# Kernel tuning notes

Hardware: AMD Instinct MI355X
Metric: run time of the kernel (lower is better)

The kernel has to match this reference:

```python
import jax, jax.numpy as jnp
import numpy as np

N_LAYERS, B, H, D = 24, 16, 32, 64
E = H * D            # 2048
TS_H = 32            # token_shift_hidden_dim
N_BRANCH = 5         # key, receptance, decay, value, bonus
GN_EPS = 1e-3        # keras GroupNormalization default epsilon


def setup_inputs() -> dict:
    key = jax.random.key(0)
    ks = jax.random.split(key, 20)
    s = 0.02
    return {
        "inputs": jax.random.normal(ks[0], (B, E), jnp.float32),
        "state": jax.random.normal(ks[1], (N_LAYERS, 1, B, E), jnp.float32),
        "state_matrix": jax.random.normal(ks[2], (N_LAYERS, B, H, D, D), jnp.float32),
        # stacked branch params, order: key, receptance, decay, value, bonus
        "mus": jax.random.normal(ks[3], (N_BRANCH, E), jnp.float32) * s,
        "lambdas": jax.random.normal(ks[4], (N_BRANCH, E), jnp.float32) * s,
        "Aw": jax.random.normal(ks[5], (N_BRANCH, E, TS_H), jnp.float32) * s,
        "Ab": jnp.zeros((N_BRANCH, TS_H), jnp.float32),
        "Bw": jax.random.normal(ks[6], (N_BRANCH, TS_H, E), jnp.float32) * s,
        "Bb": jnp.zeros((N_BRANCH, E), jnp.float32),
        "MW": jax.random.normal(ks[7], (N_BRANCH, H, D, D), jnp.float32) * s,
        "Mb": jnp.zeros((N_BRANCH, H, D), jnp.float32),
        "gate_mu": jax.random.normal(ks[8], (E,), jnp.float32) * s,
        "gate_W": jax.random.normal(ks[9], (E, E), jnp.float32) * s,
        "gate_b": jnp.zeros((E,), jnp.float32),
        "gn_gamma": jnp.ones((E,), jnp.float32),
        "gn_beta": jnp.zeros((E,), jnp.float32),
        "out_W": jax.random.normal(ks[10], (E, E), jnp.float32) * s,
        "out_b": jnp.zeros((E,), jnp.float32),
        "layer_id": 12,
    }


def reference(inputs, state, state_matrix, mus, lambdas, Aw, Ab, Bw, Bb, MW, Mb,
              gate_mu, gate_W, gate_b, gn_gamma, gn_beta, out_W, out_b, layer_id):
    x = inputs                       # [B, E]
    last_x = state[layer_id, 0]      # [B, E]
    diff = x - last_x

    # ddlerp token shift for all 5 branches at once:
    # lora(x + diff*mu) = lambda + tanh(. @ A) @ B ; out = x + lora * diff
    lora_in = x[None] + diff[None] * mus[:, None]                      # [5, B, E]
    hdn = jnp.tanh(jnp.einsum('sbe,seh->sbh', lora_in, Aw) + Ab[:, None])
    lora = jnp.einsum('sbh,she->sbe', hdn, Bw) + Bb[:, None] + lambdas[:, None]
    ts = (lora * diff[None] + x[None]).reshape(N_BRANCH, B, H, D)      # [5, B, H, D]

    # per-head dense for each branch
    proj = jnp.einsum('sbhd,shde->sbhe', ts, MW) + Mb[:, None]         # [5, B, H, D]
    k, r, w_raw, v, u = proj[0], proj[1], proj[2], proj[3], proj[4]

    g = (x * gate_mu + last_x * (1.0 - gate_mu)) @ gate_W + gate_b     # [B, E]

    kv = k[..., :, None] * v[..., None, :]                             # [B, H, D, D]
    w = jnp.exp(-jnp.exp(w_raw))[..., None]                            # [B, H, D, 1]
    S = state_matrix[layer_id]                                         # [B, H, D, D]
    wkv = kv * u[..., None] + S
    new_S = w * S + kv
    rwkv = jnp.einsum('bhij,bhj->bhi', wkv, r)                         # [B, H, D]

    # group norm: num_heads groups over channel axis
    mean = rwkv.mean(-1, keepdims=True)
    var = rwkv.var(-1, keepdims=True)
    normed = ((rwkv - mean) / jnp.sqrt(var + GN_EPS)).reshape(B, E)
    normed = normed * gn_gamma + gn_beta

    time_mixed = (normed * jax.nn.silu(g)) @ out_W + out_b             # [B, E]

    new_state = state.at[layer_id, 0].set(inputs)
    new_state_matrix = state_matrix.at[layer_id].set(new_S)
    return time_mixed, new_state, new_state_matrix
```

## Files before the change

### kernel.cpp

```cpp
#include <hip/hip_runtime.h>
#include <math.h>

#define NL 24
#define BB 16
#define HH 32
#define DD 64
#define EE 2048
#define TSH 32
#define NB 5
#define BE (BB*EE)
#define STATE_N (NL*BB*EE)
#define SM_N (NL*BB*HH*DD*DD)
#define GN_EPS 1e-3f

__global__ void k_prep(const float4* __restrict__ state4, const float4* __restrict__ inputs4,
                       float4* __restrict__ out4, const int* __restrict__ lid_p,
                       float* __restrict__ out_tm, float* __restrict__ g,
                       const float* __restrict__ out_b, const float* __restrict__ gate_b) {
    int blk = blockIdx.x, tid = threadIdx.x;
    if (blk < 768) {
        int i = blk * 256 + tid;
        int lid = *lid_p;
        int lo = lid * (BE / 4);
        float4 v = (i >= lo && i < lo + BE / 4) ? inputs4[i - lo] : state4[i];
        out4[i] = v;
    } else {
        int idx = (blk - 768) * 256 + tid;
        if (idx < BE) out_tm[idx] = out_b[idx & (EE - 1)];
        else g[idx - BE] = gate_b[(idx - BE) & (EE - 1)];
    }
}

__global__ void k_hdn(const float* __restrict__ inputs, const float* __restrict__ state,
                      const float* __restrict__ mus, const float* __restrict__ Aw,
                      const float* __restrict__ Ab, float* __restrict__ hdn,
                      const int* __restrict__ lid_p) {
    int s = blockIdx.x / BB, b = blockIdx.x % BB;
    int tid = threadIdx.x;
    int lid = *lid_p;
    __shared__ float li[EE];
    const float* x  = inputs + b * EE;
    const float* lx = state + lid * BE + b * EE;
    const float* mu = mus + s * EE;
    for (int e = tid; e < EE; e += 256) {
        float xv = x[e];
        li[e] = xv + (xv - lx[e]) * mu[e];
    }
    __syncthreads();
    int h = tid & 31, part = tid >> 5;
    const float* A = Aw + s * EE * TSH;
    float acc = 0.f;
    int e0 = part * 256;
    for (int e = e0; e < e0 + 256; ++e) acc += li[e] * A[e * TSH + h];
    __shared__ float red[32][9];
    red[h][part] = acc;
    __syncthreads();
    if (tid < 32) {
        float sum = Ab[s * TSH + tid];
        #pragma unroll
        for (int p = 0; p < 8; ++p) sum += red[tid][p];
        hdn[(s * BB + b) * TSH + tid] = tanhf(sum);
    }
}

__global__ void k_ts(const float* __restrict__ inputs, const float* __restrict__ state,
                     const float* __restrict__ lambdas, const float* __restrict__ Bw,
                     const float* __restrict__ Bb, const float* __restrict__ hdn,
                     const float* __restrict__ gate_mu, float* __restrict__ ts,
                     float* __restrict__ gx, const int* __restrict__ lid_p) {
    int idx = blockIdx.x * 256 + threadIdx.x;
    int s = idx / BE, r = idx % BE;
    int b = r / EE, e = r % EE;
    int lid = *lid_p;
    const float* hp = hdn + (s * BB + b) * TSH;
    const float* Bp = Bw + s * TSH * EE + e;
    float acc = Bb[s * EE + e] + lambdas[s * EE + e];
    #pragma unroll
    for (int h = 0; h < TSH; ++h) acc += hp[h] * Bp[h * EE];
    float xv = inputs[r];
    float lxv = state[lid * BE + r];
    ts[idx] = acc * (xv - lxv) + xv;
    if (s == 0) {
        float gm = gate_mu[e];
        gx[r] = xv * gm + lxv * (1.f - gm);
    }
}

__global__ void k_proj(const float* __restrict__ ts, const float* __restrict__ MW,
                       const float* __restrict__ Mb, float* __restrict__ proj) {
    int bi = blockIdx.x;
    int s = bi / (BB * 8);
    int r = bi % (BB * 8);
    int b = r / 8, hg = r % 8;
    int q = threadIdx.x >> 6, e = threadIdx.x & 63;
    int h = hg * 4 + q;
    __shared__ float tl[4][DD];
    tl[q][e] = ts[((s * BB + b) * HH + h) * DD + e];
    __syncthreads();
    const float* M = MW + (s * HH + h) * DD * DD;
    float acc = Mb[(s * HH + h) * DD + e];
    #pragma unroll 8
    for (int d = 0; d < DD; ++d) acc += tl[q][d] * M[d * DD + e];
    proj[((s * BB + b) * HH + h) * DD + e] = acc;
}

__global__ void k_mm(const float* __restrict__ Arows, const float* __restrict__ W,
                     float* out) {
    int et = blockIdx.x & 15, kc = blockIdx.x >> 4;
    int e = et * 128 + threadIdx.x;
    int k0 = kc * 64;
    float acc[BB];
    #pragma unroll
    for (int b = 0; b < BB; ++b) acc[b] = 0.f;
    #pragma unroll 4
    for (int kk = 0; kk < 64; ++kk) {
        float wv = W[(k0 + kk) * EE + e];
        #pragma unroll
        for (int b = 0; b < BB; ++b) acc[b] += Arows[b * EE + k0 + kk] * wv;
    }
    #pragma unroll
    for (int b = 0; b < BB; ++b) atomicAdd(&out[b * EE + e], acc[b]);
}

__global__ void k_sm_rwkv(const float4* __restrict__ sm4, float4* __restrict__ out4,
                          const float* __restrict__ proj, const float* __restrict__ g,
                          const float* __restrict__ gn_gamma, const float* __restrict__ gn_beta,
                          float* __restrict__ a_out, const int* __restrict__ lid_p) {
    int blk = blockIdx.x;
    int tid = threadIdx.x;
    int lid = *lid_p;
    int layer = blk / (BB * HH);
    int base4 = blk * (DD * DD / 4);
    if (layer != lid) {
        const float4* src = sm4 + base4;
        float4* dst = out4 + base4;
        #pragma unroll
        for (int p = 0; p < 4; ++p) dst[p * 256 + tid] = src[p * 256 + tid];
        return;
    }
    int r = blk % (BB * HH);
    int b = r / HH, h = r % HH;
    int j = tid & 63, q = tid >> 6;
    const float* P = proj + (b * HH + h) * DD + j;
    float kv   = P[0 * BE];
    float rv   = P[1 * BE];
    float wraw = P[2 * BE];
    float vv   = P[3 * BE];
    float uv   = P[4 * BE];
    float wv = expf(-expf(wraw));
    float vr = vv * rv;
    #pragma unroll
    for (int o = 32; o; o >>= 1) vr += __shfl_xor(vr, o);
    __shared__ float rw[DD];
    const float* S = (const float*)(sm4 + base4);
    float* NS = (float*)(out4 + base4);
    for (int ii = 0; ii < 16; ii += 4) {
        int i0 = q * 16 + ii;
        float sv[4], kk[4], ww[4], uu[4], pp[4];
        #pragma unroll
        for (int t = 0; t < 4; ++t) {
            sv[t] = S[(i0 + t) * DD + j];
            kk[t] = __shfl(kv, i0 + t);
            ww[t] = __shfl(wv, i0 + t);
            uu[t] = __shfl(uv, i0 + t);
        }
        #pragma unroll
        for (int t = 0; t < 4; ++t) {
            NS[(i0 + t) * DD + j] = ww[t] * sv[t] + kk[t] * vv;
            pp[t] = sv[t] * rv;
        }
        #pragma unroll
        for (int o = 32; o; o >>= 1) {
            #pragma unroll
            for (int t = 0; t < 4; ++t) pp[t] += __shfl_xor(pp[t], o);
        }
        if (j == 0) {
            #pragma unroll
            for (int t = 0; t < 4; ++t) rw[i0 + t] = kk[t] * uu[t] * vr + pp[t];
        }
    }
    __syncthreads();
    if (tid < DD) {
        float x = rw[tid];
        float m = x;
        #pragma unroll
        for (int o = 32; o; o >>= 1) m += __shfl_xor(m, o);
        m *= (1.f / 64.f);
        float d = x - m;
        float var = d * d;
        #pragma unroll
        for (int o = 32; o; o >>= 1) var += __shfl_xor(var, o);
        var *= (1.f / 64.f);
        float normed = d * rsqrtf(var + GN_EPS);
        int e = h * DD + tid;
        float ng = normed * gn_gamma[e] + gn_beta[e];
        float gval = g[b * EE + e];
        float silu = gval / (1.f + expf(-gval));
        a_out[b * EE + e] = ng * silu;
    }
}

extern "C" void kernel_launch(void* const* d_in, const int* in_sizes, int n_in,
                              void* d_out, int out_size, void* d_ws, size_t ws_size,
                              hipStream_t stream) {
    const float* inputs   = (const float*)d_in[0];
    const float* state    = (const float*)d_in[1];
    const float* sm       = (const float*)d_in[2];
    const float* mus      = (const float*)d_in[3];
    const float* lambdas  = (const float*)d_in[4];
    const float* Aw       = (const float*)d_in[5];
    const float* Ab       = (const float*)d_in[6];
    const float* Bw       = (const float*)d_in[7];
    const float* Bb       = (const float*)d_in[8];
    const float* MW       = (const float*)d_in[9];
    const float* Mb       = (const float*)d_in[10];
    const float* gate_mu  = (const float*)d_in[11];
    const float* gate_W   = (const float*)d_in[12];
    const float* gate_b   = (const float*)d_in[13];
    const float* gn_gamma = (const float*)d_in[14];
    const float* gn_beta  = (const float*)d_in[15];
    const float* out_W    = (const float*)d_in[16];
    const float* out_b    = (const float*)d_in[17];
    const int*   lid      = (const int*)d_in[18];

    float* out_tm    = (float*)d_out;
    float* out_state = out_tm + BE;
    float* out_sm    = out_state + STATE_N;

    float* ws   = (float*)d_ws;
    float* ts   = ws;
    float* proj = ts + NB * BE;
    float* hdn  = proj + NB * BE;
    float* gx   = hdn + NB * BB * TSH;
    float* g    = gx + BE;
    float* a    = g + BE;

    k_prep<<<1024, 256, 0, stream>>>((const float4*)state, (const float4*)inputs,
                                     (float4*)out_state, lid, out_tm, g, out_b, gate_b);
    k_hdn<<<NB * BB, 256, 0, stream>>>(inputs, state, mus, Aw, Ab, hdn, lid);
    k_ts<<<(NB * BE) / 256, 256, 0, stream>>>(inputs, state, lambdas, Bw, Bb, hdn,
                                              gate_mu, ts, gx, lid);
    k_proj<<<NB * BB * 8, 256, 0, stream>>>(ts, MW, Mb, proj);
    k_mm<<<512, 128, 0, stream>>>(gx, gate_W, g);
    k_sm_rwkv<<<NL * BB * HH, 256, 0, stream>>>(
        (const float4*)sm, (float4*)out_sm, proj, g, gn_gamma, gn_beta, a, lid);
    k_mm<<<512, 128, 0, stream>>>(a, out_W, out_tm);
}
```

Measured before the change: 442.4 us.

## Fuse seven launches into three and overlap state copy with matmuls

Merges the hdn, token-shift and per-head projection stages into a single per-(branch,batch) block inside the head kernel, keeping the intermediates in shared memory. The gate matmul now runs inside the same launch as the active-layer RWKV update. The bulk copy of the 23 untouched state-matrix layers moves into the tail launch beside the output matmul, and SiLU gating moves into that matmul's shared-memory staging of A. The matmuls also stage the activation rows in LDS. This removes launch gaps and lets the big memory copy overlap compute, but the fused head stage runs only 80 blocks doing serial work.

Measured after the change: 470.5 us. +6.3%, slower.

```diff
diff --git a/kernel.cpp b/kernel.cpp
--- a/kernel.cpp
+++ b/kernel.cpp
@@ -13,133 +13,136 @@
 #define SM_N (NL*BB*HH*DD*DD)
 #define GN_EPS 1e-3f
 
-__global__ void k_prep(const float4* __restrict__ state4, const float4* __restrict__ inputs4,
-                       float4* __restrict__ out4, const int* __restrict__ lid_p,
-                       float* __restrict__ out_tm, float* __restrict__ g,
-                       const float* __restrict__ out_b, const float* __restrict__ gate_b) {
+__global__ __launch_bounds__(256) void k_head(
+    const float4* __restrict__ state4, const float4* __restrict__ inputs4,
+    float4* __restrict__ out_state4,
+    float* __restrict__ out_tm, float* __restrict__ g,
+    const float* __restrict__ out_b, const float* __restrict__ gate_b,
+    const float* __restrict__ inputs, const float* __restrict__ state,
+    const float* __restrict__ mus, const float* __restrict__ Aw,
+    const float* __restrict__ Ab, const float* __restrict__ lambdas,
+    const float* __restrict__ Bw, const float* __restrict__ Bb,
+    const float* __restrict__ MW, const float* __restrict__ Mb,
+    const float* __restrict__ gate_mu, float* __restrict__ proj,
+    float* __restrict__ gx, const int* __restrict__ lid_p)
+{
     int blk = blockIdx.x, tid = threadIdx.x;
+    int lid = *lid_p;
     if (blk < 768) {
         int i = blk * 256 + tid;
-        int lid = *lid_p;
         int lo = lid * (BE / 4);
         float4 v = (i >= lo && i < lo + BE / 4) ? inputs4[i - lo] : state4[i];
-        out4[i] = v;
-    } else {
+        out_state4[i] = v;
+        return;
+    }
+    if (blk < 1024) {
         int idx = (blk - 768) * 256 + tid;
         if (idx < BE) out_tm[idx] = out_b[idx & (EE - 1)];
         else g[idx - BE] = gate_b[(idx - BE) & (EE - 1)];
-    }
-}
-
-__global__ void k_hdn(const float* __restrict__ inputs, const float* __restrict__ state,
-                      const float* __restrict__ mus, const float* __restrict__ Aw,
-                      const float* __restrict__ Ab, float* __restrict__ hdn,
-                      const int* __restrict__ lid_p) {
-    int s = blockIdx.x / BB, b = blockIdx.x % BB;
-    int tid = threadIdx.x;
-    int lid = *lid_p;
-    __shared__ float li[EE];
+        return;
+    }
+    int sb = blk - 1024;
+    int s = sb / BB, b = sb % BB;
+    __shared__ float xs[EE], dsh[EE], lis[EE], tsl[EE];
+    __shared__ float red[TSH][9];
+    __shared__ float hdnl[TSH];
     const float* x  = inputs + b * EE;
     const float* lx = state + lid * BE + b * EE;
     const float* mu = mus + s * EE;
     for (int e = tid; e < EE; e += 256) {
-        float xv = x[e];
-        li[e] = xv + (xv - lx[e]) * mu[e];
-    }
-    __syncthreads();
-    int h = tid & 31, part = tid >> 5;
-    const float* A = Aw + s * EE * TSH;
-    float acc = 0.f;
-    int e0 = part * 256;
-    for (int e = e0; e < e0 + 256; ++e) acc += li[e] * A[e * TSH + h];
-    __shared__ float red[32][9];
-    red[h][part] = acc;
-    __syncthreads();
-    if (tid < 32) {
+        float xv = x[e], lxv = lx[e];
+        float d = xv - lxv;
+        xs[e] = xv; dsh[e] = d;
+        lis[e] = xv + d * mu[e];
+        if (s == 0) {
+            float gm = gate_mu[e];
+            gx[b * EE + e] = xv * gm + lxv * (1.f - gm);
+        }
+    }
+    __syncthreads();
+    {
+        int h = tid & 31, part = tid >> 5;
+        const float* A = Aw + s * EE * TSH;
+        float acc = 0.f;
+        int e0 = part * 256;
+        #pragma unroll 8
+        for (int e = e0; e < e0 + 256; ++e) acc += lis[e] * A[e * TSH + h];
+        red[h][part] = acc;
+    }
+    __syncthreads();
+    if (tid < TSH) {
         float sum = Ab[s * TSH + tid];
         #pragma unroll
         for (int p = 0; p < 8; ++p) sum += red[tid][p];
-        hdn[(s * BB + b) * TSH + tid] = tanhf(sum);
-    }
-}
-
-__global__ void k_ts(const float* __restrict__ inputs, const float* __restrict__ state,
-                     const float* __restrict__ lambdas, const float* __restrict__ Bw,
-                     const float* __restrict__ Bb, const float* __restrict__ hdn,
-                     const float* __restrict__ gate_mu, float* __restrict__ ts,
-                     float* __restrict__ gx, const int* __restrict__ lid_p) {
-    int idx = blockIdx.x * 256 + threadIdx.x;
-    int s = idx / BE, r = idx % BE;
-    int b = r / EE, e = r % EE;
-    int lid = *lid_p;
-    const float* hp = hdn + (s * BB + b) * TSH;
-    const float* Bp = Bw + s * TSH * EE + e;
-    float acc = Bb[s * EE + e] + lambdas[s * EE + e];
-    #pragma unroll
-    for (int h = 0; h < TSH; ++h) acc += hp[h] * Bp[h * EE];
-    float xv = inputs[r];
-    float lxv = state[lid * BE + r];
-    ts[idx] = acc * (xv - lxv) + xv;
-    if (s == 0) {
-        float gm = gate_mu[e];
-        gx[r] = xv * gm + lxv * (1.f - gm);
-    }
-}
-
-__global__ void k_proj(const float* __restrict__ ts, const float* __restrict__ MW,
-                       const float* __restrict__ Mb, float* __restrict__ proj) {
-    int bi = blockIdx.x;
-    int s = bi / (BB * 8);
-    int r = bi % (BB * 8);
-    int b = r / 8, hg = r % 8;
-    int q = threadIdx.x >> 6, e = threadIdx.x & 63;
-    int h = hg * 4 + q;
-    __shared__ float tl[4][DD];
-    tl[q][e] = ts[((s * BB + b) * HH + h) * DD + e];
-    __syncthreads();
-    const float* M = MW + (s * HH + h) * DD * DD;
-    float acc = Mb[(s * HH + h) * DD + e];
+        hdnl[tid] = tanhf(sum);
+    }
+    __syncthreads();
+    for (int e = tid; e < EE; e += 256) {
+        const float* Bp = Bw + s * TSH * EE + e;
+        float acc = Bb[s * EE + e] + lambdas[s * EE + e];
+        #pragma unroll
+        for (int h2 = 0; h2 < TSH; ++h2) acc += hdnl[h2] * Bp[h2 * EE];
+        tsl[e] = acc * dsh[e] + xs[e];
+    }
+    __syncthreads();
+    for (int o = tid; o < EE; o += 256) {
+        int h2 = o >> 6, e = o & 63;
+        const float* M = MW + (s * HH + h2) * DD * DD;
+        const float* t = tsl + h2 * DD;
+        float acc = Mb[(s * HH + h2) * DD + e];
+        #pragma unroll 8
+        for (int d = 0; d < DD; ++d) acc += t[d] * M[d * DD + e];
+        proj[(s * BB + b) * EE + o] = acc;
+    }
+}
+
+template <bool SILU>
+__device__ __forceinline__ void mm_block(
+    int blk, const float* __restrict__ Arows, const float* __restrict__ Grows,
+    const float* __restrict__ W, float* __restrict__ out)
+{
+    int tid = threadIdx.x;
+    int et = blk & 7, kc = blk >> 3;
+    int e = et * 256 + tid;
+    int k0 = kc * 64;
+    __shared__ float As[BB][64];
+    for (int i = tid; i < BB * 64; i += 256) {
+        int b = i >> 6, kk = i & 63;
+        float av = Arows[b * EE + k0 + kk];
+        if constexpr (SILU) {
+            float gv = Grows[b * EE + k0 + kk];
+            av *= gv / (1.f + expf(-gv));
+        }
+        As[b][kk] = av;
+    }
+    __syncthreads();
+    float acc[BB];
+    #pragma unroll
+    for (int b = 0; b < BB; ++b) acc[b] = 0.f;
     #pragma unroll 8
-    for (int d = 0; d < DD; ++d) acc += tl[q][d] * M[d * DD + e];
-    proj[((s * BB + b) * HH + h) * DD + e] = acc;
-}
-
-__global__ void k_mm(const float* __restrict__ Arows, const float* __restrict__ W,
-                     float* out) {
-    int et = blockIdx.x & 15, kc = blockIdx.x >> 4;
-    int e = et * 128 + threadIdx.x;
-    int k0 = kc * 64;
-    float acc[BB];
-    #pragma unroll
-    for (int b = 0; b < BB; ++b) acc[b] = 0.f;
-    #pragma unroll 4
     for (int kk = 0; kk < 64; ++kk) {
         float wv = W[(k0 + kk) * EE + e];
         #pragma unroll
-        for (int b = 0; b < BB; ++b) acc[b] += Arows[b * EE + k0 + kk] * wv;
+        for (int b = 0; b < BB; ++b) acc[b] += As[b][kk] * wv;
     }
     #pragma unroll
     for (int b = 0; b < BB; ++b) atomicAdd(&out[b * EE + e], acc[b]);
 }
 
-__global__ void k_sm_rwkv(const float4* __restrict__ sm4, float4* __restrict__ out4,
-                          const float* __restrict__ proj, const float* __restrict__ g,
-                          const float* __restrict__ gn_gamma, const float* __restrict__ gn_beta,
-                          float* __restrict__ a_out, const int* __restrict__ lid_p) {
-    int blk = blockIdx.x;
-    int tid = threadIdx.x;
+__global__ __launch_bounds__(256) void k_mid(
+    const float* __restrict__ gx, const float* __restrict__ gate_W,
+    float* __restrict__ g,
+    const float4* __restrict__ sm4, float4* __restrict__ out_sm4,
+    const float* __restrict__ proj,
+    const float* __restrict__ gn_gamma, const float* __restrict__ gn_beta,
+    float* __restrict__ a_out, const int* __restrict__ lid_p)
+{
+    int blk = blockIdx.x, tid = threadIdx.x;
+    if (blk < 256) { mm_block<false>(blk, gx, nullptr, gate_W, g); return; }
     int lid = *lid_p;
-    int layer = blk / (BB * HH);
-    int base4 = blk * (DD * DD / 4);
-    if (layer != lid) {
-        const float4* src = sm4 + base4;
-        float4* dst = out4 + base4;
-        #pragma unroll
-        for (int p = 0; p < 4; ++p) dst[p * 256 + tid] = src[p * 256 + tid];
-        return;
-    }
-    int r = blk % (BB * HH);
+    int r = blk - 256;
     int b = r / HH, h = r % HH;
+    int base4 = (lid * BB * HH + r) * (DD * DD / 4);
     int j = tid & 63, q = tid >> 6;
     const float* P = proj + (b * HH + h) * DD + j;
     float kv   = P[0 * BE];
@@ -153,7 +156,7 @@
     for (int o = 32; o; o >>= 1) vr += __shfl_xor(vr, o);
     __shared__ float rw[DD];
     const float* S = (const float*)(sm4 + base4);
-    float* NS = (float*)(out4 + base4);
+    float* NS = (float*)(out_sm4 + base4);
     for (int ii = 0; ii < 16; ii += 4) {
         int i0 = q * 16 + ii;
         float sv[4], kk[4], ww[4], uu[4], pp[4];
@@ -181,23 +184,39 @@
     }
     __syncthreads();
     if (tid < DD) {
-        float x = rw[tid];
-        float m = x;
+        float xv = rw[tid];
+        float m = xv;
         #pragma unroll
         for (int o = 32; o; o >>= 1) m += __shfl_xor(m, o);
         m *= (1.f / 64.f);
-        float d = x - m;
+        float d = xv - m;
         float var = d * d;
         #pragma unroll
         for (int o = 32; o; o >>= 1) var += __shfl_xor(var, o);
         var *= (1.f / 64.f);
         float normed = d * rsqrtf(var + GN_EPS);
         int e = h * DD + tid;
-        float ng = normed * gn_gamma[e] + gn_beta[e];
-        float gval = g[b * EE + e];
-        float silu = gval / (1.f + expf(-gval));
-        a_out[b * EE + e] = ng * silu;
-    }
+        a_out[b * EE + e] = normed * gn_gamma[e] + gn_beta[e];
+    }
+}
+
+__global__ __launch_bounds__(256) void k_tail(
+    const float* __restrict__ a, const float* __restrict__ g,
+    const float* __restrict__ out_W, float* __restrict__ out_tm,
+    const float4* __restrict__ sm4, float4* __restrict__ out_sm4,
+    const int* __restrict__ lid_p)
+{
+    int blk = blockIdx.x, tid = threadIdx.x;
+    if (blk < 256) { mm_block<true>(blk, a, g, out_W, out_tm); return; }
+    int lid = *lid_p;
+    int c = blk - 256;
+    int l = c >> 9;
+    int rr = c & 511;
+    int ls = l + (l >= lid);
+    const float4* src = sm4 + ((long)ls * 512 + rr) * 1024;
+    float4* dst = out_sm4 + ((long)ls * 512 + rr) * 1024;
+    #pragma unroll
+    for (int p = 0; p < 4; ++p) dst[p * 256 + tid] = src[p * 256 + tid];
 }
 
 extern "C" void kernel_launch(void* const* d_in, const int* in_sizes, int n_in,
@@ -228,21 +247,17 @@
     float* out_sm    = out_state + STATE_N;
 
     float* ws   = (float*)d_ws;
-    float* ts   = ws;
-    float* proj = ts + NB * BE;
-    float* hdn  = proj + NB * BE;
-    float* gx   = hdn + NB * BB * TSH;
+    float* proj = ws;
+    float* gx   = proj + NB * BE;
     float* g    = gx + BE;
     float* a    = g + BE;
 
-    k_prep<<<1024, 256, 0, stream>>>((const float4*)state, (const float4*)inputs,
-                                     (float4*)out_state, lid, out_tm, g, out_b, gate_b);
-    k_hdn<<<NB * BB, 256, 0, stream>>>(inputs, state, mus, Aw, Ab, hdn, lid);
-    k_ts<<<(NB * BE) / 256, 256, 0, stream>>>(inputs, state, lambdas, Bw, Bb, hdn,
-                                              gate_mu, ts, gx, lid);
-    k_proj<<<NB * BB * 8, 256, 0, stream>>>(ts, MW, Mb, proj);
-    k_mm<<<512, 128, 0, stream>>>(gx, gate_W, g);
-    k_sm_rwkv<<<NL * BB * HH, 256, 0, stream>>>(
-        (const float4*)sm, (float4*)out_sm, proj, g, gn_gamma, gn_beta, a, lid);
-    k_mm<<<512, 128, 0, stream>>>(a, out_W, out_tm);
-}
+    k_head<<<1104, 256, 0, stream>>>((const float4*)state, (const float4*)inputs,
+                                     (float4*)out_state, out_tm, g, out_b, gate_b,
+                                     inputs, state, mus, Aw, Ab, lambdas, Bw, Bb,
+                                     MW, Mb, gate_mu, proj, gx, lid);
+    k_mid<<<768, 256, 0, stream>>>(gx, gate_W, g, (const float4*)sm, (float4*)out_sm,
+                                   proj, gn_gamma, gn_beta, a, lid);
+    k_tail<<<12032, 256, 0, stream>>>(a, g, out_W, out_tm,
+                                      (const float4*)sm, (float4*)out_sm, lid);
+}
```
